# Optimization experiments

Hardware: AMD Instinct MI355X
Metric: run time of the kernel (lower is better)

Reference implementation:

```python
import jax, jax.numpy as jnp
import numpy as np

SEQ, D_IN, D_OUT = 8192, 1024, 1024


def setup_inputs() -> dict:
    key = jax.random.key(0)
    kx, kq, kk, kv = jax.random.split(key, 4)
    # torch nn.Linear weights have shape (out_features, in_features)
    s = 1.0 / np.sqrt(D_IN)
    return {
        "x": jax.random.normal(kx, (SEQ, D_IN), dtype=jnp.float32),
        "Wq": jax.random.uniform(kq, (D_OUT, D_IN), dtype=jnp.float32, minval=-s, maxval=s),
        "Wk": jax.random.uniform(kk, (D_OUT, D_IN), dtype=jnp.float32, minval=-s, maxval=s),
        "Wv": jax.random.uniform(kv, (D_OUT, D_IN), dtype=jnp.float32, minval=-s, maxval=s),
    }


def reference(x, Wq, Wk, Wv):
    # Linear (no bias): y = x @ W.T
    q = x @ Wq.T          # [S, D_OUT]
    k = x @ Wk.T          # [S, D_OUT]
    v = x @ Wv.T          # [S, D_OUT]
    scale = 1.0 / jnp.sqrt(jnp.asarray(k.shape[-1], dtype=x.dtype))
    scores = (q @ k.T) * scale            # [S, S]
    weights = jax.nn.softmax(scores, axis=-1)
    return weights @ v                    # [S, D_OUT]
```

## Files before the change

kernel.cpp:

```cpp
#include <hip/hip_runtime.h>
#include <hip/hip_bf16.h>
#include <stdint.h>


#define SEQ 8192
#define DMODEL 1024
#define LOG2E 1.44269504088896340736f
#define GROUP_M 8

typedef __bf16 bf16_t;
typedef __bf16 bf16x8 __attribute__((ext_vector_type(8)));
typedef float f32x4 __attribute__((ext_vector_type(4)));

__global__ __launch_bounds__(256)
void convert_f32_bf16(const float* __restrict__ in, bf16_t* __restrict__ out, long n) {
    long i = ((long)blockIdx.x * 256 + threadIdx.x) * 4;
    if (i + 3 < n) {
        const float4 v = *(const float4*)(in + i);
        union { ushort4 u; bf16_t b[4]; } p;
        p.b[0] = (bf16_t)v.x; p.b[1] = (bf16_t)v.y;
        p.b[2] = (bf16_t)v.z; p.b[3] = (bf16_t)v.w;
        *(ushort4*)(out + i) = p.u;
    }
}

__global__ __launch_bounds__(256)
void add_f32(float* __restrict__ out, const float* __restrict__ part, long n) {
    long i = ((long)blockIdx.x * 256 + threadIdx.x) * 4;
    if (i + 3 < n) {
        float4 a = *(const float4*)(out + i);
        const float4 b = *(const float4*)(part + i);
        a.x += b.x; a.y += b.y; a.z += b.z; a.w += b.w;
        *(float4*)(out + i) = a;
    }
}

__global__ __launch_bounds__(256)
void zero_f32(float* __restrict__ p, int n) {
    int i = blockIdx.x * 256 + threadIdx.x;
    if (i < n) p[i] = 0.0f;
}

template <typename OutT, int MODE>
__global__ __launch_bounds__(256, 3)
void gemm_nt(const bf16_t* __restrict__ A, const bf16_t* __restrict__ B,
             OutT* __restrict__ C0, OutT* __restrict__ C1,
             float* __restrict__ lsum,
             int M, int N, int Kps, int lda, int ldb, int ldc,
             long plane, int cshift, float alpha)
{
    __shared__ bf16_t As[128 * 32];
    __shared__ bf16_t Bs[128 * 32];

    const int tid  = threadIdx.x;
    const int wave = tid >> 6;
    const int lane = tid & 63;

    const int nbm = M >> 7, nbn = N >> 7;
    const int tiles = nbm * nbn;
    int bid = blockIdx.x;
    const int sid = bid / tiles;
    bid -= sid * tiles;
    const long kbase = (long)sid * Kps;
    OutT* __restrict__ C = sid ? C1 : C0;

    const int cpx = tiles >> 3;
    bid = (bid & 7) * cpx + (bid >> 3);

    const int per_group = GROUP_M * nbn;
    const int gid   = bid / per_group;
    const int rem   = bid - gid * per_group;
    const int first = gid * GROUP_M;
    const int gsz   = min(nbm - first, GROUP_M);
    const int bm    = first + rem % gsz;
    const int bn    = rem / gsz;
    const long row0 = (long)bm * 128;
    const long col0 = (long)bn * 128;

    const int wm = (wave >> 1) * 64;
    const int wn = (wave & 1) * 64;
    const int lr = lane & 15;
    const int lq = lane >> 4;

    const int rt = tid >> 2;
    const int sl = ((tid & 3) + ((tid >> 3) & 3)) & 3;
    const bf16_t* pa = A + (row0 + rt) * (long)lda + kbase + sl * 8;
    const bf16_t* pb = B + (col0 + rt) * (long)ldb + kbase + sl * 8;

    const int p0  = (lq - ((lr >> 1) & 3)) & 3;
    const int oA  = (wm + lr) * 32 + p0 * 8;
    const int oB  = (wn + lr) * 32 + p0 * 8;

    f32x4 acc[4][4] = {};

    for (int k0 = 0; k0 < Kps; k0 += 32) {
        #pragma unroll
        for (int i = 0; i < 2; ++i) {
            const bf16_t* ga = pa + k0 + (long)i * 64 * lda;
            const bf16_t* gb = pb + k0 + (long)i * 64 * ldb;
            __builtin_amdgcn_global_load_lds(
                (const __attribute__((address_space(1))) uint32_t*)ga,
                (__attribute__((address_space(3))) uint32_t*)(As + (long)(i * 256 + tid) * 8),
                16, 0, 0);
            __builtin_amdgcn_global_load_lds(
                (const __attribute__((address_space(1))) uint32_t*)gb,
                (__attribute__((address_space(3))) uint32_t*)(Bs + (long)(i * 256 + tid) * 8),
                16, 0, 0);
        }
        __syncthreads();

        bf16x8 af[4], bfr[4];
        #pragma unroll
        for (int mi = 0; mi < 4; ++mi)
            af[mi] = *(const bf16x8*)(As + oA + mi * 512);
        #pragma unroll
        for (int ni = 0; ni < 4; ++ni)
            bfr[ni] = *(const bf16x8*)(Bs + oB + ni * 512);
        #pragma unroll
        for (int mi = 0; mi < 4; ++mi)
            #pragma unroll
            for (int ni = 0; ni < 4; ++ni)
                acc[mi][ni] = __builtin_amdgcn_mfma_f32_16x16x32_bf16(
                    af[mi], bfr[ni], acc[mi][ni], 0, 0, 0);
        __syncthreads();
    }

    OutT* __restrict__ Cb = C + (col0 >> cshift) * plane;
    const int ccol0 = (int)(col0 & (((long)1 << cshift) - 1));

    if (MODE == 1) {
        #pragma unroll
        for (int mi = 0; mi < 4; ++mi)
            #pragma unroll
            for (int rg = 0; rg < 4; ++rg) {
                const long r = row0 + wm + mi * 16 + lq * 4 + rg;
                float part = 0.f;
                #pragma unroll
                for (int ni = 0; ni < 4; ++ni) {
                    const int c = ccol0 + wn + ni * 16 + lr;
                    const float e = exp2f(alpha * acc[mi][ni][rg]);
                    part += e;
                    Cb[r * (long)ldc + c] = (OutT)e;
                }
                part += __shfl_xor(part, 1);
                part += __shfl_xor(part, 2);
                part += __shfl_xor(part, 4);
                part += __shfl_xor(part, 8);
                if (lr == 0) atomicAdd(&lsum[r], part);
            }
    } else if (MODE == 2) {
        #pragma unroll
        for (int mi = 0; mi < 4; ++mi)
            #pragma unroll
            for (int rg = 0; rg < 4; ++rg) {
                const long r = row0 + wm + mi * 16 + lq * 4 + rg;
                const float inv = 1.0f / lsum[r];
                #pragma unroll
                for (int ni = 0; ni < 4; ++ni) {
                    const int c = ccol0 + wn + ni * 16 + lr;
                    Cb[r * (long)ldc + c] = (OutT)(acc[mi][ni][rg] * inv);
                }
            }
    } else {
        #pragma unroll
        for (int mi = 0; mi < 4; ++mi)
            #pragma unroll
            for (int ni = 0; ni < 4; ++ni)
                #pragma unroll
                for (int rg = 0; rg < 4; ++rg) {
                    const long r = row0 + wm + mi * 16 + lq * 4 + rg;
                    const int  c = ccol0 + wn + ni * 16 + lr;
                    Cb[r * (long)ldc + c] = (OutT)(alpha * acc[mi][ni][rg]);
                }
    }
}

__global__ __launch_bounds__(256)
void transpose_bf16(const bf16_t* __restrict__ in, bf16_t* __restrict__ out,
                    int R, int ldin, int ldout)
{
    __shared__ bf16_t tile[32][33];
    const int tx = threadIdx.x & 31;
    const int ty = threadIdx.x >> 5;
    const int c0 = blockIdx.x * 32;
    const int r0 = blockIdx.y * 32;
    #pragma unroll
    for (int j = 0; j < 32; j += 8)
        tile[ty + j][tx] = in[(long)(r0 + ty + j) * ldin + c0 + tx];
    __syncthreads();
    #pragma unroll
    for (int j = 0; j < 32; j += 8)
        out[(long)(c0 + ty + j) * ldout + r0 + tx] = tile[tx][ty + j];
}

extern "C" void kernel_launch(void* const* d_in, const int* in_sizes, int n_in,
                              void* d_out, int out_size, void* d_ws, size_t ws_size,
                              hipStream_t stream)
{
    const float* x  = (const float*)d_in[0];
    const float* Wq = (const float*)d_in[1];
    const float* Wk = (const float*)d_in[2];
    const float* Wv = (const float*)d_in[3];
    float* out = (float*)d_out;

    char* ws = (char*)d_ws;
    const long XN = (long)SEQ * DMODEL;
    const long WN = (long)DMODEL * DMODEL;
    const long SN = (long)SEQ * SEQ;

    bf16_t* xb   = (bf16_t*)ws;
    bf16_t* wcat = (bf16_t*)(ws + XN * 2);
    bf16_t* qb   = (bf16_t*)(ws + XN * 2 + WN * 6);
    bf16_t* kb   = qb + XN;
    bf16_t* vb   = qb + 2 * XN;
    bf16_t* Sb   = (bf16_t*)(ws + XN * 2 + WN * 6 + XN * 6);
    float*  pvp  = (float*)(ws + XN * 2 + WN * 6 + XN * 6 + SN * 2);
    float*  lsum = (float*)(ws + XN * 2 + WN * 6 + XN * 6 + SN * 2 + XN * 4);
    bf16_t* vtb  = xb;

    const size_t base_need = (size_t)(XN * 2 + WN * 6 + XN * 6 + SN * 2);
    const bool use_split = ws_size >= base_need + XN * 4 + SEQ * 4;
    if (!use_split) lsum = (float*)(ws + base_need);

    convert_f32_bf16<<<(int)(XN / 4 / 256), 256, 0, stream>>>(x,  xb, XN);
    convert_f32_bf16<<<(int)(WN / 4 / 256), 256, 0, stream>>>(Wq, wcat,          WN);
    convert_f32_bf16<<<(int)(WN / 4 / 256), 256, 0, stream>>>(Wk, wcat + WN,     WN);
    convert_f32_bf16<<<(int)(WN / 4 / 256), 256, 0, stream>>>(Wv, wcat + 2 * WN, WN);
    zero_f32<<<SEQ / 256, 256, 0, stream>>>(lsum, SEQ);

    dim3 blk(256);
    gemm_nt<bf16_t, 0><<<(SEQ / 128) * (3 * DMODEL / 128), blk, 0, stream>>>(
        xb, wcat, qb, qb, nullptr, SEQ, 3 * DMODEL, DMODEL,
        DMODEL, DMODEL, DMODEL, XN, 10, 1.0f);

    transpose_bf16<<<dim3(DMODEL / 32, SEQ / 32), blk, 0, stream>>>(
        vb, vtb, SEQ, DMODEL, SEQ);

    gemm_nt<bf16_t, 1><<<(SEQ / 128) * (SEQ / 128), blk, 0, stream>>>(
        qb, kb, Sb, Sb, lsum, SEQ, SEQ, DMODEL,
        DMODEL, DMODEL, SEQ, 0, 30, 0.03125f * LOG2E);

    if (use_split) {
        gemm_nt<float, 2><<<2 * (SEQ / 128) * (DMODEL / 128), blk, 0, stream>>>(
            Sb, vtb, out, pvp, lsum, SEQ, DMODEL, SEQ / 2,
            SEQ, SEQ, DMODEL, 0, 30, 1.0f);
        add_f32<<<(int)(XN / 4 / 256), 256, 0, stream>>>(out, pvp, XN);
    } else {
        gemm_nt<float, 2><<<(SEQ / 128) * (DMODEL / 128), blk, 0, stream>>>(
            Sb, vtb, out, out, lsum, SEQ, DMODEL, SEQ,
            SEQ, SEQ, DMODEL, 0, 30, 1.0f);
    }
}
```

Before: 503.4 us.

## Add 128x256 K64 GEMM kernel for QKV projection and PV products

New measurement: 460.8 us (median of 2 runs). 1.09x faster.

```diff
diff --git a/kernel.cpp b/kernel.cpp
--- a/kernel.cpp
+++ b/kernel.cpp
@@ -42,12 +42,137 @@
 }
 
 template <typename OutT, int MODE>
-__global__ __launch_bounds__(256, 3)
-void gemm_nt(const bf16_t* __restrict__ A, const bf16_t* __restrict__ B,
+__global__ __launch_bounds__(512, 2)
+void gemm_hn(const bf16_t* __restrict__ A, const bf16_t* __restrict__ B,
              OutT* __restrict__ C0, OutT* __restrict__ C1,
              float* __restrict__ lsum,
              int M, int N, int Kps, int lda, int ldb, int ldc,
              long plane, int cshift, float alpha)
+{
+    __shared__ bf16_t As[128 * 64];
+    __shared__ bf16_t Bs[256 * 64];
+
+    const int tid  = threadIdx.x;
+    const int wave = tid >> 6;
+    const int lane = tid & 63;
+
+    const int nbm = M >> 7, nbn = N >> 8;
+    const int tiles = nbm * nbn;
+    int bid = blockIdx.x;
+    const int sid = bid / tiles;
+    bid -= sid * tiles;
+    const long kbase = (long)sid * Kps;
+    OutT* __restrict__ C = sid ? C1 : C0;
+
+    const int cpx = tiles >> 3;
+    bid = (bid & 7) * cpx + (bid >> 3);
+
+    const int per_group = GROUP_M * nbn;
+    const int gid   = bid / per_group;
+    const int rem   = bid - gid * per_group;
+    const int first = gid * GROUP_M;
+    const int gsz   = min(nbm - first, GROUP_M);
+    const int bm    = first + rem % gsz;
+    const int bn    = rem / gsz;
+    const long row0 = (long)bm * 128;
+    const long col0 = (long)bn * 256;
+
+    const int wm = (wave >> 2) * 64;
+    const int wn = (wave & 3) * 64;
+    const int lr = lane & 15;
+    const int lq = lane >> 4;
+
+    const int rt = tid >> 3;
+    const int sl = ((tid & 7) + rt) & 7;
+    const bf16_t* pa = A + (row0 + rt) * (long)lda + kbase + sl * 8;
+    const bf16_t* pb = B + (col0 + rt) * (long)ldb + kbase + sl * 8;
+
+    const int p0  = (lq - lr) & 7;
+    const int p1  = p0 ^ 4;
+    const int oA0 = (wm + lr) * 64 + p0 * 8;
+    const int oA1 = (wm + lr) * 64 + p1 * 8;
+    const int oB0 = (wn + lr) * 64 + p0 * 8;
+    const int oB1 = (wn + lr) * 64 + p1 * 8;
+
+    f32x4 acc[4][4] = {};
+
+    for (int k0 = 0; k0 < Kps; k0 += 64) {
+        #pragma unroll
+        for (int i = 0; i < 2; ++i) {
+            const bf16_t* ga = pa + k0 + (long)i * 64 * lda;
+            __builtin_amdgcn_global_load_lds(
+                (const __attribute__((address_space(1))) uint32_t*)ga,
+                (__attribute__((address_space(3))) uint32_t*)(As + i * 4096 + tid * 8),
+                16, 0, 0);
+        }
+        #pragma unroll
+        for (int i = 0; i < 4; ++i) {
+            const bf16_t* gb = pb + k0 + (long)i * 64 * ldb;
+            __builtin_amdgcn_global_load_lds(
+                (const __attribute__((address_space(1))) uint32_t*)gb,
+                (__attribute__((address_space(3))) uint32_t*)(Bs + i * 4096 + tid * 8),
+                16, 0, 0);
+        }
+        __syncthreads();
+
+        #pragma unroll
+        for (int t = 0; t < 2; ++t) {
+            bf16x8 af[4], bfr[4];
+            const int oA = t ? oA1 : oA0;
+            const int oB = t ? oB1 : oB0;
+            #pragma unroll
+            for (int mi = 0; mi < 4; ++mi)
+                af[mi] = *(const bf16x8*)(As + oA + mi * 1024);
+            #pragma unroll
+            for (int ni = 0; ni < 4; ++ni)
+                bfr[ni] = *(const bf16x8*)(Bs + oB + ni * 1024);
+            #pragma unroll
+            for (int mi = 0; mi < 4; ++mi)
+                #pragma unroll
+                for (int ni = 0; ni < 4; ++ni)
+                    acc[mi][ni] = __builtin_amdgcn_mfma_f32_16x16x32_bf16(
+                        af[mi], bfr[ni], acc[mi][ni], 0, 0, 0);
+        }
+        __syncthreads();
+    }
+
+    OutT* __restrict__ Cb = C + (col0 >> cshift) * plane;
+    const int ccol0 = (int)(col0 & (((long)1 << cshift) - 1));
+
+    if (MODE == 2) {
+        #pragma unroll
+        for (int mi = 0; mi < 4; ++mi)
+            #pragma unroll
+            for (int rg = 0; rg < 4; ++rg) {
+                const long r = row0 + wm + mi * 16 + lq * 4 + rg;
+                const float inv = 1.0f / lsum[r];
+                #pragma unroll
+                for (int ni = 0; ni < 4; ++ni) {
+                    const int c = ccol0 + wn + ni * 16 + lr;
+                    Cb[r * (long)ldc + c] = (OutT)(acc[mi][ni][rg] * inv);
+                }
+            }
+    } else {
+        #pragma unroll
+        for (int mi = 0; mi < 4; ++mi)
+            #pragma unroll
+            for (int ni = 0; ni < 4; ++ni)
+                #pragma unroll
+                for (int rg = 0; rg < 4; ++rg) {
+                    const long r = row0 + wm + mi * 16 + lq * 4 + rg;
+                    const int  c = ccol0 + wn + ni * 16 + lr;
+                    Cb[r * (long)ldc + c] = (OutT)(alpha * acc[mi][ni][rg]);
+                }
+    }
+}
+
+template <typename OutT, int MODE>
+__global__ __launch_bounds__(256, 3)
+void gemm32(const bf16_t* __restrict__ A, const bf16_t* __restrict__ B,
+            OutT* __restrict__ C0, OutT* __restrict__ C1,
+            float* __restrict__ lsum,
+            int M, int N, int Kps, int lda, int ldb, int ldc,
+            long plane, int cshift, float alpha)
 {
     __shared__ bf16_t As[128 * 32];
     __shared__ bf16_t Bs[128 * 32];
@@ -228,25 +353,26 @@
     convert_f32_bf16<<<(int)(WN / 4 / 256), 256, 0, stream>>>(Wv, wcat + 2 * WN, WN);
     zero_f32<<<SEQ / 256, 256, 0, stream>>>(lsum, SEQ);
 
-    dim3 blk(256);
-    gemm_nt<bf16_t, 0><<<(SEQ / 128) * (3 * DMODEL / 128), blk, 0, stream>>>(
+    dim3 blk256(256);
+    dim3 blk512(512);
+    gemm_hn<bf16_t, 0><<<(SEQ / 128) * (3 * DMODEL / 256), blk512, 0, stream>>>(
         xb, wcat, qb, qb, nullptr, SEQ, 3 * DMODEL, DMODEL,
         DMODEL, DMODEL, DMODEL, XN, 10, 1.0f);
 
-    transpose_bf16<<<dim3(DMODEL / 32, SEQ / 32), blk, 0, stream>>>(
+    transpose_bf16<<<dim3(DMODEL / 32, SEQ / 32), blk256, 0, stream>>>(
         vb, vtb, SEQ, DMODEL, SEQ);
 
-    gemm_nt<bf16_t, 1><<<(SEQ / 128) * (SEQ / 128), blk, 0, stream>>>(
+    gemm32<bf16_t, 1><<<(SEQ / 128) * (SEQ / 128), blk256, 0, stream>>>(
         qb, kb, Sb, Sb, lsum, SEQ, SEQ, DMODEL,
         DMODEL, DMODEL, SEQ, 0, 30, 0.03125f * LOG2E);
 
     if (use_split) {
-        gemm_nt<float, 2><<<2 * (SEQ / 128) * (DMODEL / 128), blk, 0, stream>>>(
+        gemm_hn<float, 2><<<2 * (SEQ / 128) * (DMODEL / 256), blk512, 0, stream>>>(
             Sb, vtb, out, pvp, lsum, SEQ, DMODEL, SEQ / 2,
             SEQ, SEQ, DMODEL, 0, 30, 1.0f);
         add_f32<<<(int)(XN / 4 / 256), 256, 0, stream>>>(out, pvp, XN);
     } else {
-        gemm_nt<float, 2><<<(SEQ / 128) * (DMODEL / 128), blk, 0, stream>>>(
+        gemm_hn<float, 2><<<(SEQ / 128) * (DMODEL / 256), blk512, 0, stream>>>(
             Sb, vtb, out, out, lsum, SEQ, DMODEL, SEQ,
             SEQ, SEQ, DMODEL, 0, 30, 1.0f);
     }
```
